# Kernel tuning notes

Hardware: AMD Instinct MI355X
Metric: run time of the kernel (lower is better)

## Reference

```python
import jax, jax.numpy as jnp
import numpy as np

K_SIGN = 100000.0   # tanh sharpness approximating sign()
EPS = 1e-05         # acos clamp epsilon


def setup_inputs() -> dict:
    key = jax.random.key(0)
    B, N, KV = 2, 8, 64
    contour = jax.random.uniform(key, (B, N, KV, 2), dtype=jnp.float32)  # values in [0,1]
    return {"contour": contour, "size": 128}


def reference(contour, size):
    b, n, kv, _ = contour.shape
    dt = contour.dtype
    # pixel grid, normalized by size (matches torch meshgrid 'ij' + reshape(-1,2)/size)
    g = jnp.arange(size, dtype=dt)
    mesh = jnp.stack(jnp.meshgrid(g, g, indexing="ij"), axis=-1).reshape(-1, 2) / size  # (S2, 2)

    c = contour.reshape(b * n, 1, kv, 2)          # (bn, 1, kv, 2)
    diff = c - mesh[None, :, None, :]             # (bn, S2, kv, 2)
    roll_diff = jnp.roll(diff, -1, axis=2)        # next vertex

    # sign = diff * swap(roll_diff); sign[...,1]-sign[...,0] = d_y*rd_x - d_x*rd_y
    cross = diff[..., 1] * roll_diff[..., 0] - diff[..., 0] * roll_diff[..., 1]
    sign = jnp.tanh(K_SIGN * cross)               # (bn, S2, kv)

    norm_diff = jnp.linalg.norm(diff, axis=3)
    norm_roll = jnp.linalg.norm(roll_diff, axis=3)
    scalar = jnp.sum(diff * roll_diff, axis=3)
    cosang = jnp.clip(scalar / (norm_diff * norm_roll), -1.0 + EPS, 1.0 - EPS)
    angles = jnp.arccos(cosang)                   # (bn, S2, kv)

    sum_angles = jnp.clip(jnp.abs(jnp.sum(sign * angles, axis=2) / (2.0 * jnp.pi)), 0.0, 1.0)
    return sum_angles.reshape(b, n, size, size)
```

## Files before the change

### kernel.cpp

```cpp
#include <hip/hip_runtime.h>
#include <math.h>

#define BLOCK 256
#define SPLIT 4
#define PPT   2
#define MAX_KV_LDS 1024

__device__ __forceinline__ float rcp1(float x)  { return __builtin_amdgcn_rcpf(x); }
__device__ __forceinline__ float rsq1(float x)  { return __builtin_amdgcn_rsqf(x); }
__device__ __forceinline__ float sqrt1(float x) { return __builtin_amdgcn_sqrtf(x); }

#define ACONST 4.4721439e-3f
#define PIF    3.14159265358979f
#define PImA   3.1371205f
#define TWOPI  6.28318530717959f
#define INV2PI 0.15915494309189535f
#define K1     2.000040e-5f
#define CR2MIN 1.6e-9f

__device__ __forceinline__ float rare_fix(float cr, float dt)
{
    float z   = cr * rcp1(dt);
    float c1  = copysignf(ACONST, z) - z;
    bool  f1  = cr * cr < K1 * (dt * dt);
    float c1a = f1 ? c1 : 0.0f;
    float ac = fabsf(cr), ad = fabsf(dt);
    float mn = fminf(ac, ad), mx = fmaxf(ac, ad);
    float q  = mn * rcp1(mx);
    float s2 = q * q;
    float r = fmaf(fmaf(fmaf(fmaf(0.0208351f, s2, -0.0851330f), s2,
                  0.1801410f), s2, -0.3302995f), s2, 0.9998660f) * q;
    r = (ac > ad) ? (1.57079632679f - r) : r;
    float theta = (dt < 0.0f) ? (PIF - r) : r;
    float thc = __builtin_amdgcn_fmed3f(theta, ACONST, PImA);
    float t  = cr * 100000.0f;
    float s  = t * t;
    float nm = t * fmaf(s + 105.0f, s, 945.0f);
    float qd = fmaf(fmaf(15.0f, s, 420.0f), s, 945.0f);
    float th = __builtin_amdgcn_fmed3f(nm * rcp1(qd), -1.0f, 1.0f);
    float scr = (cr >= 0.0f) ? 1.0f : -1.0f;
    return fmaf(th, thc, -scr * theta) - c1a;
}

__device__ __forceinline__ float edge_term_s(float cr, float dt)
{
    float n2 = fmaf(cr, cr, dt * dt);
    float co = dt * rsq1(n2);
    co = __builtin_amdgcn_fmed3f(co, -0.99999f, 0.99999f);
    float y = fabsf(co);
    float p = fmaf(fmaf(fmaf(-0.0187293f, y, 0.0742610f), y, -0.2121144f),
                   y, 1.5707288f);
    float a = sqrt1(1.0f - y) * p;
    a = (co >= 0.0f) ? a : (PIF - a);
    float t  = cr * 100000.0f;
    float s  = t * t;
    float nm = t * fmaf(s + 105.0f, s, 945.0f);
    float qd = fmaf(fmaf(15.0f, s, 420.0f), s, 945.0f);
    float th = __builtin_amdgcn_fmed3f(nm * rcp1(qd), -1.0f, 1.0f);
    return th * a;
}

__global__ __launch_bounds__(BLOCK, 4)
void contour_mask_kernel(const float2* __restrict__ contour,
                         const int* __restrict__ size_ptr,
                         float* __restrict__ out,
                         int out_size, int in0_elems)
{
    __shared__ float2 verts[MAX_KV_LDS + 1];

    const int size     = *size_ptr;
    const int S2       = size * size;
    const int bn_total = out_size / S2;
    const int kv       = in0_elems / (bn_total * 2);

    const int tid  = threadIdx.x;
    const int PIX_PER_BLOCK = (BLOCK / SPLIT) * PPT;
    const int base = blockIdx.x * PIX_PER_BLOCK;

    const int bn0 = base / S2;
    const int rem = base - bn0 * S2;
    const bool one_image = (rem + PIX_PER_BLOCK <= S2) &&
                           (base + PIX_PER_BLOCK <= out_size);
    const bool use_lds = (kv <= MAX_KV_LDS) && one_image;

    if (use_lds) {
        for (int i = tid; i < kv; i += BLOCK)
            verts[i] = contour[(size_t)bn0 * kv + i];
        if (tid == 0)
            verts[kv] = contour[(size_t)bn0 * kv];
    }
    __syncthreads();

    const int seg = tid & (SPLIT - 1);
    const float inv_size = 1.0f / (float)size;

    if (use_lds && kv == 64 && (size & 1) == 0) {
        const int pi0 = rem / size;
        const int pj0 = rem - pi0 * size;
        const int t   = (tid / SPLIT) * PPT;

        int pjA = pj0 + t, piA = pi0;
        while (pjA >= size) { pjA -= size; ++piA; }

        const float mx  = (float)piA * inv_size;
        const float myA = (float)pjA * inv_size;

        const int k0 = seg * 16;
        float2 v = verts[k0];
        float dx  = v.x - mx;
        float dyA = v.y - myA;
        float dyB = dyA - inv_size;
        bool dygtA = dyA > 0.0f;
        bool dygtB = dyB > 0.0f;
        float SA = 0.0f, SB = 0.0f;
        bool anyA = false, anyB = false;

        #pragma unroll
        for (int k = 0; k < 16; ++k) {
            float2 vn = verts[k0 + k + 1];
            float rx  = vn.x - mx;
            float ryA = vn.y - myA;
            float ryB = ryA - inv_size;
            float P   = dx * rx;

            {
                float cr = fmaf(dyA, rx, -(dx * ryA));
                float dt = fmaf(dyA, ryA, P);
                bool rygt = ryA > 0.0f;
                float dS = 0.0f;
                dS = (!dygtA && rygt && cr < 0.0f) ? -TWOPI : dS;
                dS = ( dygtA && !rygt && cr > 0.0f) ?  TWOPI : dS;
                float z  = cr * rcp1(dt);
                float c1 = copysignf(ACONST, z) - z;
                float cr2 = cr * cr;
                bool f1 = cr2 < K1 * (dt * dt);
                SA += dS + (f1 ? c1 : 0.0f);
                anyA = anyA || (cr2 < CR2MIN);
                dyA = ryA; dygtA = rygt;
            }
            {
                float cr = fmaf(dyB, rx, -(dx * ryB));
                float dt = fmaf(dyB, ryB, P);
                bool rygt = ryB > 0.0f;
                float dS = 0.0f;
                dS = (!dygtB && rygt && cr < 0.0f) ? -TWOPI : dS;
                dS = ( dygtB && !rygt && cr > 0.0f) ?  TWOPI : dS;
                float z  = cr * rcp1(dt);
                float c1 = copysignf(ACONST, z) - z;
                float cr2 = cr * cr;
                bool f1 = cr2 < K1 * (dt * dt);
                SB += dS + (f1 ? c1 : 0.0f);
                anyB = anyB || (cr2 < CR2MIN);
                dyB = ryB; dygtB = rygt;
            }
            dx = rx;
        }

        if (__ballot(anyA || anyB)) {
            float2 v0 = verts[k0];
            float dx2  = v0.x - mx;
            float dA   = v0.y - myA;
            float dB   = dA - inv_size;
            for (int k = 0; k < 16; ++k) {
                float2 vn = verts[k0 + k + 1];
                float rx  = vn.x - mx;
                float rA  = vn.y - myA;
                float rB  = rA - inv_size;
                if (anyA) {
                    float cr = fmaf(dA, rx, -(dx2 * rA));
                    if (cr * cr < CR2MIN) {
                        float dt = fmaf(dx2, rx, dA * rA);
                        SA += rare_fix(cr, dt);
                    }
                }
                if (anyB) {
                    float cr = fmaf(dB, rx, -(dx2 * rB));
                    if (cr * cr < CR2MIN) {
                        float dt = fmaf(dx2, rx, dB * rB);
                        SB += rare_fix(cr, dt);
                    }
                }
                dx2 = rx; dA = rA; dB = rB;
            }
        }

        SA += __shfl_xor(SA, 1, 64);
        SB += __shfl_xor(SB, 1, 64);
        SA += __shfl_xor(SA, 2, 64);
        SB += __shfl_xor(SB, 2, 64);

        if (seg == 0) {
            float2 res;
            res.x = fminf(fabsf(SA) * INV2PI, 1.0f);
            res.y = fminf(fabsf(SB) * INV2PI, 1.0f);
            *(float2*)(out + base + t) = res;
        }
        return;
    }

    const int q  = (kv + SPLIT - 1) / SPLIT;
    const int k0 = min(seg * q, kv);
    const int k1 = min(k0 + q, kv);

    #pragma unroll
    for (int px = 0; px < PPT; ++px) {
        const int pixel = base + (tid / SPLIT) * PPT + px;
        float a = 0.0f;
        if (pixel < out_size && k0 < k1) {
            const int bn = pixel / S2;
            const int p  = pixel - bn * S2;
            const int pi = p / size;
            const int pj = p - pi * size;
            const float mxs = pi * inv_size;
            const float mys = pj * inv_size;
            const float2* vsrc = contour + (size_t)bn * kv;
            float2 v = vsrc[k0];
            float dx = v.x - mxs, dy = v.y - mys;
            for (int k = k0; k < k1; ++k) {
                int kn = k + 1; if (kn == kv) kn = 0;
                float2 vn = vsrc[kn];
                float rx = vn.x - mxs, ry = vn.y - mys;
                float cr = fmaf(dy, rx, -(dx * ry));
                float dt = fmaf(dx, rx, dy * ry);
                a += edge_term_s(cr, dt);
                dx = rx; dy = ry;
            }
        }
        a += __shfl_xor(a, 1, 64);
        a += __shfl_xor(a, 2, 64);
        if (pixel < out_size && seg == 0)
            out[pixel] = fminf(fabsf(a) * INV2PI, 1.0f);
    }
}

extern "C" void kernel_launch(void* const* d_in, const int* in_sizes, int n_in,
                              void* d_out, int out_size, void* d_ws, size_t ws_size,
                              hipStream_t stream)
{
    const float2* contour  = (const float2*)d_in[0];
    const int*    size_ptr = (const int*)d_in[1];
    float*        out      = (float*)d_out;

    const int PIX_PER_BLOCK = (BLOCK / SPLIT) * PPT;
    const int blocks = (out_size + PIX_PER_BLOCK - 1) / PIX_PER_BLOCK;
    contour_mask_kernel<<<blocks, BLOCK, 0, stream>>>(
        contour, size_ptr, out, out_size, in_sizes[0]);
}
```

Baseline: 69.30 us.

## Drop small-angle correction term and halve vertex split to two segments

Removes the per-edge small-angle correction (the rcp and c1 term) from the hot winding-number loop, so each edge only needs the cross product and crossing test. The small-cross-product fix-up path keeps its exact handling. The vertex split drops from 4 to 2 segments of 32 edges, halving the shuffle reduction and doubling per-thread work. The LDS fast path is also selected by an integer kv==64 check with shift/mask indexing for power-of-two sizes. The change drops a correction term that was previously applied to every edge, so it risks accuracy, and it halves the block count, which lowers parallelism.

```diff
diff --git a/kernel.cpp b/kernel.cpp
--- a/kernel.cpp
+++ b/kernel.cpp
@@ -2,7 +2,7 @@
 #include <math.h>
 
 #define BLOCK 256
-#define SPLIT 4
+#define SPLIT 2
 #define PPT   2
 #define MAX_KV_LDS 1024
 
@@ -15,15 +15,10 @@
 #define PImA   3.1371205f
 #define TWOPI  6.28318530717959f
 #define INV2PI 0.15915494309189535f
-#define K1     2.000040e-5f
 #define CR2MIN 1.6e-9f
 
 __device__ __forceinline__ float rare_fix(float cr, float dt)
 {
-    float z   = cr * rcp1(dt);
-    float c1  = copysignf(ACONST, z) - z;
-    bool  f1  = cr * cr < K1 * (dt * dt);
-    float c1a = f1 ? c1 : 0.0f;
     float ac = fabsf(cr), ad = fabsf(dt);
     float mn = fminf(ac, ad), mx = fmaxf(ac, ad);
     float q  = mn * rcp1(mx);
@@ -39,7 +34,7 @@
     float qd = fmaf(fmaf(15.0f, s, 420.0f), s, 945.0f);
     float th = __builtin_amdgcn_fmed3f(nm * rcp1(qd), -1.0f, 1.0f);
     float scr = (cr >= 0.0f) ? 1.0f : -1.0f;
-    return fmaf(th, thc, -scr * theta) - c1a;
+    return fmaf(th, thc, -scr * theta);
 }
 
 __device__ __forceinline__ float edge_term_s(float cr, float dt)
@@ -68,10 +63,8 @@
 {
     __shared__ float2 verts[MAX_KV_LDS + 1];
 
-    const int size     = *size_ptr;
-    const int S2       = size * size;
-    const int bn_total = out_size / S2;
-    const int kv       = in0_elems / (bn_total * 2);
+    const int size = *size_ptr;
+    const int S2   = size * size;
 
     const int tid  = threadIdx.x;
     const int PIX_PER_BLOCK = (BLOCK / SPLIT) * PPT;
@@ -81,22 +74,30 @@
     const int rem = base - bn0 * S2;
     const bool one_image = (rem + PIX_PER_BLOCK <= S2) &&
                            (base + PIX_PER_BLOCK <= out_size);
-    const bool use_lds = (kv <= MAX_KV_LDS) && one_image;
+    const bool kv64 = ((long long)in0_elems * S2 == 128LL * out_size);
+    const bool use_lds = kv64 && one_image;
 
     if (use_lds) {
-        for (int i = tid; i < kv; i += BLOCK)
-            verts[i] = contour[(size_t)bn0 * kv + i];
+        for (int i = tid; i < 64; i += BLOCK)
+            verts[i] = contour[(size_t)bn0 * 64 + i];
         if (tid == 0)
-            verts[kv] = contour[(size_t)bn0 * kv];
+            verts[64] = contour[(size_t)bn0 * 64];
     }
     __syncthreads();
 
-    const int seg = tid & (SPLIT - 1);
     const float inv_size = 1.0f / (float)size;
 
-    if (use_lds && kv == 64 && (size & 1) == 0) {
-        const int pi0 = rem / size;
-        const int pj0 = rem - pi0 * size;
+    if (use_lds && (size & 1) == 0) {
+        int pi0, pj0;
+        if ((size & (size - 1)) == 0) {
+            const int lg = 31 - __clz(size);
+            pi0 = rem >> lg;
+            pj0 = rem & (size - 1);
+        } else {
+            pi0 = rem / size;
+            pj0 = rem - pi0 * size;
+        }
+        const int seg = tid & (SPLIT - 1);
         const int t   = (tid / SPLIT) * PPT;
 
         int pjA = pj0 + t, piA = pi0;
@@ -105,7 +106,7 @@
         const float mx  = (float)piA * inv_size;
         const float myA = (float)pjA * inv_size;
 
-        const int k0 = seg * 16;
+        const int k0 = seg * 32;
         float2 v = verts[k0];
         float dx  = v.x - mx;
         float dyA = v.y - myA;
@@ -116,52 +117,41 @@
         bool anyA = false, anyB = false;
 
         #pragma unroll
-        for (int k = 0; k < 16; ++k) {
+        for (int k = 0; k < 32; ++k) {
             float2 vn = verts[k0 + k + 1];
             float rx  = vn.x - mx;
             float ryA = vn.y - myA;
             float ryB = ryA - inv_size;
-            float P   = dx * rx;
 
             {
                 float cr = fmaf(dyA, rx, -(dx * ryA));
-                float dt = fmaf(dyA, ryA, P);
                 bool rygt = ryA > 0.0f;
                 float dS = 0.0f;
                 dS = (!dygtA && rygt && cr < 0.0f) ? -TWOPI : dS;
                 dS = ( dygtA && !rygt && cr > 0.0f) ?  TWOPI : dS;
-                float z  = cr * rcp1(dt);
-                float c1 = copysignf(ACONST, z) - z;
-                float cr2 = cr * cr;
-                bool f1 = cr2 < K1 * (dt * dt);
-                SA += dS + (f1 ? c1 : 0.0f);
-                anyA = anyA || (cr2 < CR2MIN);
+                SA += dS;
+                anyA = anyA || (cr * cr < CR2MIN);
                 dyA = ryA; dygtA = rygt;
             }
             {
                 float cr = fmaf(dyB, rx, -(dx * ryB));
-                float dt = fmaf(dyB, ryB, P);
                 bool rygt = ryB > 0.0f;
                 float dS = 0.0f;
                 dS = (!dygtB && rygt && cr < 0.0f) ? -TWOPI : dS;
                 dS = ( dygtB && !rygt && cr > 0.0f) ?  TWOPI : dS;
-                float z  = cr * rcp1(dt);
-                float c1 = copysignf(ACONST, z) - z;
-                float cr2 = cr * cr;
-                bool f1 = cr2 < K1 * (dt * dt);
-                SB += dS + (f1 ? c1 : 0.0f);
-                anyB = anyB || (cr2 < CR2MIN);
+                SB += dS;
+                anyB = anyB || (cr * cr < CR2MIN);
                 dyB = ryB; dygtB = rygt;
             }
             dx = rx;
         }
 
-        if (__ballot(anyA || anyB)) {
+        if (anyA || anyB) {
             float2 v0 = verts[k0];
             float dx2  = v0.x - mx;
             float dA   = v0.y - myA;
             float dB   = dA - inv_size;
-            for (int k = 0; k < 16; ++k) {
+            for (int k = 0; k < 32; ++k) {
                 float2 vn = verts[k0 + k + 1];
                 float rx  = vn.x - mx;
                 float rA  = vn.y - myA;
@@ -186,8 +176,6 @@
 
         SA += __shfl_xor(SA, 1, 64);
         SB += __shfl_xor(SB, 1, 64);
-        SA += __shfl_xor(SA, 2, 64);
-        SB += __shfl_xor(SB, 2, 64);
 
         if (seg == 0) {
             float2 res;
@@ -198,9 +186,12 @@
         return;
     }
 
-    const int q  = (kv + SPLIT - 1) / SPLIT;
-    const int k0 = min(seg * q, kv);
-    const int k1 = min(k0 + q, kv);
+    const int bn_total = out_size / S2;
+    const int kv       = in0_elems / (bn_total * 2);
+    const int seg = tid & (SPLIT - 1);
+    const int q   = (kv + SPLIT - 1) / SPLIT;
+    const int k0  = min(seg * q, kv);
+    const int k1  = min(k0 + q, kv);
 
     #pragma unroll
     for (int px = 0; px < PPT; ++px) {
@@ -227,7 +218,6 @@
             }
         }
         a += __shfl_xor(a, 1, 64);
-        a += __shfl_xor(a, 2, 64);
         if (pixel < out_size && seg == 0)
             out[pixel] = fminf(fabsf(a) * INV2PI, 1.0f);
     }
```

After: 67.22 us. 3.0% less time.
